# Kernel optimization log

Hardware: AMD Instinct MI355X
Metric: run time of the kernel (lower is better)

Reference implementation:

```python
import jax, jax.numpy as jnp
import numpy as np

D_MODEL = 512
N_HEADS = 8
D_HEAD = D_MODEL // N_HEADS
EPS = 1e-5


def layer_norm(x, g, b):
    mu = jnp.mean(x, axis=-1, keepdims=True)
    var = jnp.mean(jnp.square(x - mu), axis=-1, keepdims=True)
    return (x - mu) * jax.lax.rsqrt(var + EPS) * g + b


def setup_inputs() -> dict:
    key = jax.random.key(0)
    ks = jax.random.split(key, 8)
    B, L, D = 2, 4096, D_MODEL
    x = jax.random.normal(ks[0], (B, L, D), dtype=jnp.float32)
    # monotonically increasing event timestamps (hours)
    timestamps = jnp.sort(jax.random.uniform(ks[1], (B, L), dtype=jnp.float32) * 1000.0, axis=-1)
    mask = jnp.ones((B, L), dtype=jnp.float32)
    s = 0.02
    return {
        "x": x,
        "timestamps": timestamps,
        "mask": mask,
        "ln1_g": jnp.ones((D,), jnp.float32),
        "ln1_b": jnp.zeros((D,), jnp.float32),
        "w_qkv": jax.random.normal(ks[2], (3 * D, D), jnp.float32) * s,
        "w_out": jax.random.normal(ks[3], (D, D), jnp.float32) * s,
        "decay_rate": jnp.ones((N_HEADS,), jnp.float32) * 0.01,
        "ln2_g": jnp.ones((D,), jnp.float32),
        "ln2_b": jnp.zeros((D,), jnp.float32),
        "w_ff1": jax.random.normal(ks[4], (4 * D, D), jnp.float32) * s,
        "w_ff2": jax.random.normal(ks[5], (D, 4 * D), jnp.float32) * s,
    }


def reference(x, timestamps, mask, ln1_g, ln1_b, w_qkv, w_out, decay_rate, ln2_g, ln2_b, w_ff1, w_ff2):
    B, L, D = x.shape
    H, dh = N_HEADS, D_HEAD
    scale = dh ** (-0.5)

    xn = layer_norm(x, ln1_g, ln1_b)
    qkv = (xn @ w_qkv.T).reshape(B, L, 3, H, dh).transpose(2, 0, 3, 1, 4)  # [3,B,H,L,dh]
    q, k, v = qkv[0], qkv[1], qkv[2]

    attn = jnp.einsum("bhid,bhjd->bhij", q, k) * scale  # [B,H,L,L]

    # temporal-decay bias
    t_diff = jnp.abs(timestamps[:, None, :, None] - timestamps[:, None, None, :]) / 24.0  # [B,1,L,L]
    decay = jax.nn.softplus(decay_rate)[None, :, None, None]  # [1,H,1,1]
    attn = attn - decay * t_diff

    # causal mask
    causal = jnp.triu(jnp.ones((L, L), dtype=bool), k=1)
    attn = jnp.where(causal[None, None], -jnp.inf, attn)

    # padding mask over keys
    pad = (mask == 0)[:, None, None, :]  # [B,1,1,L]
    attn = jnp.where(pad, -jnp.inf, attn)

    attn = jax.nn.softmax(attn, axis=-1)
    out = jnp.einsum("bhij,bhjd->bhid", attn, v).transpose(0, 2, 1, 3).reshape(B, L, D)

    x = x + out @ w_out.T
    h = layer_norm(x, ln2_g, ln2_b)
    x = x + jax.nn.silu(h @ w_ff1.T) @ w_ff2.T
    return x
```

## Files before the change

### kernel.cpp

```cpp
#include <hip/hip_runtime.h>
#include <hip/hip_bf16.h>
#include <cmath>


#define L_SEQ 4096
#define D_MODEL 512
#define N_HEADS 8
#define D_HEAD 64
#define QKV_LD 1536

typedef __attribute__((ext_vector_type(8))) short bf16x8;
typedef __attribute__((ext_vector_type(4))) float f32x4;
typedef __attribute__((ext_vector_type(4))) unsigned u32x4;

__device__ __forceinline__ __hip_bfloat16 f2bf(float v) { return __float2bfloat16(v); }

__device__ __forceinline__ float exp2_raw(float x) {
  float r;
  asm("v_exp_f32 %0, %1" : "=v"(r) : "v"(x));
  return r;
}

__device__ __forceinline__ void gl_lds16(const __hip_bfloat16* g, __hip_bfloat16* l) {
  __builtin_amdgcn_global_load_lds((__attribute__((address_space(1))) void*)g,
                                   (__attribute__((address_space(3))) void*)l, 16, 0, 0);
}

__global__ __launch_bounds__(256) void cvt4b_kernel(const float* __restrict__ s0, __hip_bfloat16* __restrict__ d0,
                                                    const float* __restrict__ s1, __hip_bfloat16* __restrict__ d1,
                                                    const float* __restrict__ s2, __hip_bfloat16* __restrict__ d2,
                                                    const float* __restrict__ s3, __hip_bfloat16* __restrict__ d3,
                                                    const float* __restrict__ ts,
                                                    const float* __restrict__ mask,
                                                    const float* __restrict__ decay_rate,
                                                    float* __restrict__ biasH) {
  const int i = blockIdx.x * 256 + threadIdx.x;
  if (i < 786432) {
    const float* s;
    __hip_bfloat16* d;
    int off;
    if (i < 196608) { s = s0; d = d0; off = i; }
    else if (i < 262144) { s = s1; d = d1; off = i - 196608; }
    else if (i < 524288) { s = s2; d = d2; off = i - 262144; }
    else { s = s3; d = d3; off = i - 524288; }
    const float4 v = ((const float4*)s)[off];
    d[4 * off + 0] = f2bf(v.x);
    d[4 * off + 1] = f2bf(v.y);
    d[4 * off + 2] = f2bf(v.z);
    d[4 * off + 3] = f2bf(v.w);
  } else {
    const int idx = i - 786432;
    const int col = idx & 4095;
    const int h = (idx >> 12) & 7;
    const int b = idx >> 15;
    const float LOG2E = 1.4426950408889634f;
    const float dfac = log1pf(expf(decay_rate[h])) * (1.0f / 24.0f) * LOG2E;
    const float m = mask[b * 4096 + col];
    biasH[idx] = dfac * ts[b * 4096 + col] + (m != 0.f ? 0.f : -1e30f);
  }
}

__global__ __launch_bounds__(256) void ln_kernel(const float* __restrict__ x,
                                                 const float* __restrict__ g,
                                                 const float* __restrict__ b,
                                                 __hip_bfloat16* __restrict__ out) {
  const int row = blockIdx.x;
  const int t = threadIdx.x;
  const float* xr = x + (size_t)row * D_MODEL;
  float v0 = xr[t];
  float v1 = xr[t + 256];
  float s = v0 + v1;
  float qq = v0 * v0 + v1 * v1;
  for (int off = 32; off > 0; off >>= 1) {
    s += __shfl_xor(s, off);
    qq += __shfl_xor(qq, off);
  }
  __shared__ float red[8];
  const int wid = t >> 6;
  if ((t & 63) == 0) { red[wid] = s; red[4 + wid] = qq; }
  __syncthreads();
  s = red[0] + red[1] + red[2] + red[3];
  qq = red[4] + red[5] + red[6] + red[7];
  const float mu = s * (1.0f / 512.0f);
  const float var = fmaxf(qq * (1.0f / 512.0f) - mu * mu, 0.0f);
  const float rstd = rsqrtf(var + 1e-5f);
  __hip_bfloat16* orow = out + (size_t)row * D_MODEL;
  orow[t] = f2bf((v0 - mu) * rstd * g[t] + b[t]);
  orow[t + 256] = f2bf((v1 - mu) * rstd * g[t + 256] + b[t + 256]);
}

template <int EPI>
__global__ __launch_bounds__(256) void gemm_kernel(const __hip_bfloat16* __restrict__ A,
                                                   const __hip_bfloat16* __restrict__ B,
                                                   int M, int N, int K,
                                                   __hip_bfloat16* __restrict__ vtout,
                                                   void* __restrict__ C) {
  __shared__ __align__(16) __hip_bfloat16 As[2][128 * 32];
  __shared__ __align__(16) __hip_bfloat16 Bs[2][128 * 32];
  const int tid = threadIdx.x;
  const int lane = tid & 63, w = tid >> 6;
  const int m0 = blockIdx.y * 128, n0 = blockIdx.x * 128;
  const int wm = (w >> 1) * 64, wn = (w & 1) * 64;
  const int r = lane & 15, q = lane >> 4;

  f32x4 acc[4][4];
  const f32x4 zz = {0.f, 0.f, 0.f, 0.f};
  for (int i = 0; i < 4; i++)
    for (int j = 0; j < 4; j++) acc[i][j] = zz;

  const int c0 = tid, c1 = 256 + tid;
  const int row0 = c0 >> 2, kb0 = (c0 & 3) * 8;
  const int row1 = c1 >> 2, kb1 = (c1 & 3) * 8;

#define GEMM_STAGE(k0, buf)                                                     \
  do {                                                                          \
    gl_lds16(A + (size_t)(m0 + row0) * K + ((k0) + kb0), &As[buf][c0 * 8]);     \
    gl_lds16(B + (size_t)(n0 + row0) * K + ((k0) + kb0), &Bs[buf][c0 * 8]);     \
    gl_lds16(A + (size_t)(m0 + row1) * K + ((k0) + kb1), &As[buf][c1 * 8]);     \
    gl_lds16(B + (size_t)(n0 + row1) * K + ((k0) + kb1), &Bs[buf][c1 * 8]);     \
  } while (0)

  GEMM_STAGE(0, 0);
  const int niter = K >> 5;
  for (int it = 0; it < niter; it++) {
    const int cur = it & 1;
    if (it + 1 < niter) {
      GEMM_STAGE((it + 1) << 5, cur ^ 1);
      asm volatile("s_waitcnt vmcnt(4)" ::: "memory");
    } else {
      asm volatile("s_waitcnt vmcnt(0)" ::: "memory");
    }
    __builtin_amdgcn_s_barrier();
    bf16x8 af[4], bfr[4];
    for (int mi = 0; mi < 4; mi++)
      af[mi] = *(const bf16x8*)(&As[cur][(wm + mi * 16 + r) * 32 + q * 8]);
    for (int ni = 0; ni < 4; ni++)
      bfr[ni] = *(const bf16x8*)(&Bs[cur][(wn + ni * 16 + r) * 32 + q * 8]);
    for (int mi = 0; mi < 4; mi++)
      for (int ni = 0; ni < 4; ni++)
        acc[mi][ni] = __builtin_amdgcn_mfma_f32_16x16x32_bf16(af[mi], bfr[ni], acc[mi][ni], 0, 0, 0);
    __builtin_amdgcn_s_barrier();
  }
#undef GEMM_STAGE

  for (int mi = 0; mi < 4; mi++)
    for (int ni = 0; ni < 4; ni++)
      for (int j = 0; j < 4; j++) {
        const int gm = m0 + wm + mi * 16 + q * 4 + j;
        const int gn = n0 + wn + ni * 16 + r;
        float v = acc[mi][ni][j];
        const size_t idx = (size_t)gm * N + gn;
        if (EPI == 0) {
          ((__hip_bfloat16*)C)[idx] = f2bf(v);
        } else if (EPI == 2) {
          v = v / (1.0f + expf(-v));
          ((__hip_bfloat16*)C)[idx] = f2bf(v);
        } else {
          if (n0 < 1024) {
            ((__hip_bfloat16*)C)[idx] = f2bf(v);
          } else {
            const int bb = gm >> 12, ll = gm & 4095;
            const int hd = gn - 1024;
            const int kin = ll & 63;
            const int sl = (kin & 0x23) | ((kin & 0x10) >> 2) | ((kin & 0x0c) << 1);
            vtout[(size_t)(bb * 512 + hd) * 4096 + (ll & ~63) + sl] = f2bf(v);
          }
        }
      }
}

__global__ __launch_bounds__(256) void gemm_res64_kernel(const __hip_bfloat16* __restrict__ A,
                                                         const __hip_bfloat16* __restrict__ B,
                                                         int M, int N, int K,
                                                         const float* __restrict__ aux,
                                                         float* __restrict__ C) {
  __shared__ __align__(16) __hip_bfloat16 As[2][64 * 32];
  __shared__ __align__(16) __hip_bfloat16 Bs[2][128 * 32];
  const int tid = threadIdx.x;
  const int lane = tid & 63, w = tid >> 6;
  const int m0 = blockIdx.y * 64, n0 = blockIdx.x * 128;
  const int wm = (w >> 1) * 32, wn = (w & 1) * 64;
  const int r = lane & 15, q = lane >> 4;

  f32x4 acc[2][4];
  const f32x4 zz = {0.f, 0.f, 0.f, 0.f};
  for (int i = 0; i < 2; i++)
    for (int j = 0; j < 4; j++) acc[i][j] = zz;

  const int rowA = tid >> 2, kbA = (tid & 3) * 8;
  const int c0 = tid, c1 = 256 + tid;
  const int rowB0 = c0 >> 2, kb0 = (c0 & 3) * 8;
  const int rowB1 = c1 >> 2, kb1 = (c1 & 3) * 8;

#define GEMM_STAGE64(k0, buf)                                                    \
  do {                                                                           \
    gl_lds16(A + (size_t)(m0 + rowA) * K + ((k0) + kbA), &As[buf][tid * 8]);     \
    gl_lds16(B + (size_t)(n0 + rowB0) * K + ((k0) + kb0), &Bs[buf][c0 * 8]);     \
    gl_lds16(B + (size_t)(n0 + rowB1) * K + ((k0) + kb1), &Bs[buf][c1 * 8]);     \
  } while (0)

  GEMM_STAGE64(0, 0);
  const int niter = K >> 5;
  for (int it = 0; it < niter; it++) {
    const int cur = it & 1;
    if (it + 1 < niter) {
      GEMM_STAGE64((it + 1) << 5, cur ^ 1);
      asm volatile("s_waitcnt vmcnt(3)" ::: "memory");
    } else {
      asm volatile("s_waitcnt vmcnt(0)" ::: "memory");
    }
    __builtin_amdgcn_s_barrier();
    bf16x8 af[2], bfr[4];
    for (int mi = 0; mi < 2; mi++)
      af[mi] = *(const bf16x8*)(&As[cur][(wm + mi * 16 + r) * 32 + q * 8]);
    for (int ni = 0; ni < 4; ni++)
      bfr[ni] = *(const bf16x8*)(&Bs[cur][(wn + ni * 16 + r) * 32 + q * 8]);
    for (int mi = 0; mi < 2; mi++)
      for (int ni = 0; ni < 4; ni++)
        acc[mi][ni] = __builtin_amdgcn_mfma_f32_16x16x32_bf16(af[mi], bfr[ni], acc[mi][ni], 0, 0, 0);
    __builtin_amdgcn_s_barrier();
  }
#undef GEMM_STAGE64

  for (int mi = 0; mi < 2; mi++)
    for (int ni = 0; ni < 4; ni++)
      for (int j = 0; j < 4; j++) {
        const int gm = m0 + wm + mi * 16 + q * 4 + j;
        const int gn = n0 + wn + ni * 16 + r;
        const size_t idx = (size_t)gm * N + gn;
        C[idx] = acc[mi][ni][j] + aux[idx];
      }
}

__device__ __forceinline__ void stage_kv128(int w, int lane, int key0,
                                            const __hip_bfloat16* __restrict__ Kg,
                                            const __hip_bfloat16* __restrict__ Vg,
                                            __hip_bfloat16* Ks, __hip_bfloat16* Vs) {
  const int krow_in = lane >> 3;
  const int kcs = (lane & 7) ^ krow_in;
  const int vrow_in = lane >> 4;
  const int vch = lane & 15;
#pragma unroll
  for (int ii = 0; ii < 2; ii++) {
    const int i = w * 2 + ii;
    const int krow = i * 8 + krow_in;
    gl_lds16(Kg + (size_t)(key0 + krow) * QKV_LD + kcs * 8, Ks + i * 512 + lane * 8);
    const int vrow = i * 4 + vrow_in;
    const int vcs = vch ^ (vrow & 7);
    gl_lds16(Vg + (size_t)vrow * L_SEQ + key0 + vcs * 8, Vs + i * 512 + lane * 8);
  }
}

template <bool CAUSAL>
__device__ __forceinline__ void attn_tile128(int key0, int lw0, int r, int q,
                                             const __hip_bfloat16* Ks,
                                             const __hip_bfloat16* Vs,
                                             const float* biasLds,
                                             float scale2,
                                             const bf16x8& qf0, const bf16x8& qf1,
                                             const bf16x8& onesf,
                                             f32x4* o, f32x4& ls) {
  const int r7 = r & 7;
  const f32x4 zz = {0.f, 0.f, 0.f, 0.f};
  f32x4 bias4[8];
#pragma unroll
  for (int hc = 0; hc < 8; hc++)
    bias4[hc] = *(const f32x4*)(biasLds + key0 + hc * 16 + q * 4);
  f32x4 s[8];
  __builtin_amdgcn_s_setprio(1);
#pragma unroll
  for (int hc = 0; hc < 8; hc++) {
    const __hip_bfloat16* kr = Ks + (hc * 16 + r) * 64;
    bf16x8 k0 = *(const bf16x8*)(kr + ((q ^ r7) * 8));
    bf16x8 k1 = *(const bf16x8*)(kr + (((q + 4) ^ r7) * 8));
    f32x4 a = zz;
    a = __builtin_amdgcn_mfma_f32_16x16x32_bf16(k0, qf0, a, 0, 0, 0);
    a = __builtin_amdgcn_mfma_f32_16x16x32_bf16(k1, qf1, a, 0, 0, 0);
    s[hc] = a;
  }
  __builtin_amdgcn_s_setprio(0);
  float p[8][4];
#pragma unroll
  for (int hc = 0; hc < 8; hc++)
#pragma unroll
    for (int j = 0; j < 4; j++) {
      float pv = exp2_raw(fmaf(s[hc][j], scale2, bias4[hc][j]));
      if (CAUSAL) pv = (key0 + hc * 16 + q * 4 + j <= lw0 + r) ? pv : 0.f;
      p[hc][j] = pv;
    }
  bf16x8 pa[4];
#pragma unroll
  for (int kc = 0; kc < 4; kc++) {
    u32x4 pw;
    unsigned w0, w1, w2, w3;
    asm("v_cvt_pk_bf16_f32 %0, %1, %2" : "=v"(w0) : "v"(p[2 * kc][0]), "v"(p[2 * kc][1]));
    asm("v_cvt_pk_bf16_f32 %0, %1, %2" : "=v"(w1) : "v"(p[2 * kc][2]), "v"(p[2 * kc][3]));
    asm("v_cvt_pk_bf16_f32 %0, %1, %2" : "=v"(w2) : "v"(p[2 * kc + 1][0]), "v"(p[2 * kc + 1][1]));
    asm("v_cvt_pk_bf16_f32 %0, %1, %2" : "=v"(w3) : "v"(p[2 * kc + 1][2]), "v"(p[2 * kc + 1][3]));
    pw[0] = w0; pw[1] = w1; pw[2] = w2; pw[3] = w3;
    pa[kc] = *(bf16x8*)&pw;
  }
  __builtin_amdgcn_s_setprio(1);
#pragma unroll
  for (int kc = 0; kc < 4; kc++) {
#pragma unroll
    for (int c = 0; c < 4; c++) {
      const __hip_bfloat16* vr = Vs + (c * 16 + r) * 128 + (((kc * 4 + q) ^ r7) * 8);
      bf16x8 vf = *(const bf16x8*)vr;
      o[c] = __builtin_amdgcn_mfma_f32_16x16x32_bf16(pa[kc], vf, o[c], 0, 0, 0);
    }
    ls = __builtin_amdgcn_mfma_f32_16x16x32_bf16(pa[kc], onesf, ls, 0, 0, 0);
  }
  __builtin_amdgcn_s_setprio(0);
}

__global__ __launch_bounds__(512, 4) void attn_kernel(const __hip_bfloat16* __restrict__ qkv,
                                                      const __hip_bfloat16* __restrict__ vt,
                                                      const float* __restrict__ biasH,
                                                      __hip_bfloat16* __restrict__ out) {
  const int blk = blockIdx.x;
  const int bh = blk & 15;
  const int pr = blk >> 4;
  const int b = bh >> 3, h = bh & 7;
  const int tid = threadIdx.x, lane = tid & 63, w = tid >> 6;
  const int grp = w >> 2, wg = w & 3;
  const int qi = grp ? (63 - pr) : pr;
  const int l0 = qi * 64;
  const int lw0 = l0 + wg * 16;
  const int r = lane & 15, q = lane >> 4;

  __shared__ __align__(16) __hip_bfloat16 Ksm[2][128 * 64];
  __shared__ __align__(16) __hip_bfloat16 Vsm[2][64 * 128];
  __shared__ __align__(16) float biasLds[4096];

  const float LOG2E = 1.4426950408889634f;
  const float scale2 = 0.125f * LOG2E;

  const __hip_bfloat16* Kg = qkv + (size_t)b * L_SEQ * QKV_LD + 512 + h * 64;
  const __hip_bfloat16* Vg = vt + (size_t)bh * 64 * L_SEQ;
  const float* biasHp = biasH + (size_t)bh * L_SEQ;

  stage_kv128(w, lane, 0, Kg, Vg, Ksm[0], Vsm[0]);
#pragma unroll
  for (int ii = 0; ii < 2; ii++) {
    const int fo = (w * 2 + ii) * 256;
    gl_lds16((const __hip_bfloat16*)(biasHp + fo + lane * 4),
             (__hip_bfloat16*)(biasLds + fo + lane * 4));
  }

  bf16x8 qf0, qf1;
  {
    const __hip_bfloat16* qrow = qkv + (size_t)(b * L_SEQ + lw0 + r) * QKV_LD + h * 64 + q * 8;
    qf0 = *(const bf16x8*)qrow;
    qf1 = *(const bf16x8*)(qrow + 32);
  }

  const f32x4 zz = {0.f, 0.f, 0.f, 0.f};
  f32x4 o[4];
  for (int c = 0; c < 4; c++) o[c] = zz;
  f32x4 ls = zz;

  bf16x8 onesf;
  for (int i = 0; i < 8; i++) ((short*)&onesf)[i] = (short)0x3F80;

  const int ntA = (pr >> 1) + 1;
  const int ntB = ((63 - pr) >> 1) + 1;
  const int nt = grp ? ntB : ntA;

  for (int t = 0; t < ntB; t++) {
    const int cur = t & 1;
    if (t + 1 < ntB) {
      stage_kv128(w, lane, (t + 1) << 7, Kg, Vg, Ksm[cur ^ 1], Vsm[cur ^ 1]);
      asm volatile("s_waitcnt vmcnt(4)" ::: "memory");
    } else {
      asm volatile("s_waitcnt vmcnt(0)" ::: "memory");
    }
    __builtin_amdgcn_s_barrier();
    if (t < nt) {
      if (t == nt - 1)
        attn_tile128<true>(t << 7, lw0, r, q, Ksm[cur], Vsm[cur], biasLds, scale2, qf0, qf1,
                           onesf, o, ls);
      else
        attn_tile128<false>(t << 7, lw0, r, q, Ksm[cur], Vsm[cur], biasLds, scale2, qf0, qf1,
                            onesf, o, ls);
    }
    __builtin_amdgcn_s_barrier();
  }

  float invj[4];
  for (int j = 0; j < 4; j++) invj[j] = 1.0f / ls[j];
  for (int c = 0; c < 4; c++)
    for (int j = 0; j < 4; j++) {
      const int rowg = lw0 + q * 4 + j;
      out[(size_t)(b * L_SEQ + rowg) * D_MODEL + h * 64 + c * 16 + r] = f2bf(o[c][j] * invj[j]);
    }
}

extern "C" void kernel_launch(void* const* d_in, const int* in_sizes, int n_in,
                              void* d_out, int out_size, void* d_ws, size_t ws_size,
                              hipStream_t stream) {
  const float* x = (const float*)d_in[0];
  const float* ts = (const float*)d_in[1];
  const float* mask = (const float*)d_in[2];
  const float* ln1_g = (const float*)d_in[3];
  const float* ln1_b = (const float*)d_in[4];
  const float* w_qkv = (const float*)d_in[5];
  const float* w_out = (const float*)d_in[6];
  const float* decay = (const float*)d_in[7];
  const float* ln2_g = (const float*)d_in[8];
  const float* ln2_b = (const float*)d_in[9];
  const float* w_ff1 = (const float*)d_in[10];
  const float* w_ff2 = (const float*)d_in[11];

  char* ws = (char*)d_ws;
  __hip_bfloat16* wqkv_b = (__hip_bfloat16*)(ws + 0);
  __hip_bfloat16* wout_b = (__hip_bfloat16*)(ws + 1572864);
  __hip_bfloat16* wff1_b = (__hip_bfloat16*)(ws + 2097152);
  __hip_bfloat16* wff2_b = (__hip_bfloat16*)(ws + 4194304);
  __hip_bfloat16* xn = (__hip_bfloat16*)(ws + 6291456);
  __hip_bfloat16* qkv = (__hip_bfloat16*)(ws + 14680064);
  __hip_bfloat16* attnout = (__hip_bfloat16*)(ws + 39845888);
  __hip_bfloat16* h = attnout;
  __hip_bfloat16* ff1out = (__hip_bfloat16*)(ws + 6291456);
  float* x2 = (float*)(ws + 48234496);
  float* biasH = (float*)(ws + 48234496);
  __hip_bfloat16* vt = (__hip_bfloat16*)(ws + 48496640);
  float* out = (float*)d_out;

  const int M = 2 * L_SEQ;

  cvt4b_kernel<<<dim3(3328), dim3(256), 0, stream>>>(w_qkv, wqkv_b, w_out, wout_b,
                                                     w_ff1, wff1_b, w_ff2, wff2_b,
                                                     ts, mask, decay, biasH);

  ln_kernel<<<dim3(M), dim3(256), 0, stream>>>(x, ln1_g, ln1_b, xn);
  gemm_kernel<4><<<dim3(12, 64), dim3(256), 0, stream>>>(xn, wqkv_b, M, 1536, 512, vt, qkv);
  attn_kernel<<<dim3(512), dim3(512), 0, stream>>>(qkv, vt, biasH, attnout);
  gemm_res64_kernel<<<dim3(4, 128), dim3(256), 0, stream>>>(attnout, wout_b, M, 512, 512, x, x2);
  ln_kernel<<<dim3(M), dim3(256), 0, stream>>>(x2, ln2_g, ln2_b, h);
  gemm_kernel<2><<<dim3(16, 64), dim3(256), 0, stream>>>(h, wff1_b, M, 2048, 512, nullptr, ff1out);
  gemm_res64_kernel<<<dim3(4, 128), dim3(256), 0, stream>>>(ff1out, wff2_b, M, 512, 2048, x2, out);
}
```

Before: 267.8 us.

## Triple-buffer GEMM LDS staging and fuse first layernorm into prep kernel

Both GEMM kernels move from double to triple buffering of shared-memory tiles. The next-next tile is now prefetched after the MFMA block, which cuts one barrier per iteration and leaves more time to hide global-load latency. The first layernorm is also merged into the weight-conversion and bias prep kernel as extra blocks, which removes one launch. The extra LDS may lower occupancy, and the single remaining barrier has to guard the reuse of each buffer correctly.

```diff
diff --git a/kernel.cpp b/kernel.cpp
--- a/kernel.cpp
+++ b/kernel.cpp
@@ -26,37 +26,67 @@
                                    (__attribute__((address_space(3))) void*)l, 16, 0, 0);
 }
 
-__global__ __launch_bounds__(256) void cvt4b_kernel(const float* __restrict__ s0, __hip_bfloat16* __restrict__ d0,
-                                                    const float* __restrict__ s1, __hip_bfloat16* __restrict__ d1,
-                                                    const float* __restrict__ s2, __hip_bfloat16* __restrict__ d2,
-                                                    const float* __restrict__ s3, __hip_bfloat16* __restrict__ d3,
-                                                    const float* __restrict__ ts,
-                                                    const float* __restrict__ mask,
-                                                    const float* __restrict__ decay_rate,
-                                                    float* __restrict__ biasH) {
-  const int i = blockIdx.x * 256 + threadIdx.x;
-  if (i < 786432) {
-    const float* s;
-    __hip_bfloat16* d;
-    int off;
-    if (i < 196608) { s = s0; d = d0; off = i; }
-    else if (i < 262144) { s = s1; d = d1; off = i - 196608; }
-    else if (i < 524288) { s = s2; d = d2; off = i - 262144; }
-    else { s = s3; d = d3; off = i - 524288; }
-    const float4 v = ((const float4*)s)[off];
-    d[4 * off + 0] = f2bf(v.x);
-    d[4 * off + 1] = f2bf(v.y);
-    d[4 * off + 2] = f2bf(v.z);
-    d[4 * off + 3] = f2bf(v.w);
+__global__ __launch_bounds__(256) void prep_kernel(const float* __restrict__ s0, __hip_bfloat16* __restrict__ d0,
+                                                   const float* __restrict__ s1, __hip_bfloat16* __restrict__ d1,
+                                                   const float* __restrict__ s2, __hip_bfloat16* __restrict__ d2,
+                                                   const float* __restrict__ s3, __hip_bfloat16* __restrict__ d3,
+                                                   const float* __restrict__ ts,
+                                                   const float* __restrict__ mask,
+                                                   const float* __restrict__ decay_rate,
+                                                   float* __restrict__ biasH,
+                                                   const float* __restrict__ x,
+                                                   const float* __restrict__ ln1_g,
+                                                   const float* __restrict__ ln1_b,
+                                                   __hip_bfloat16* __restrict__ xn) {
+  if (blockIdx.x < 3328) {
+    const int i = blockIdx.x * 256 + threadIdx.x;
+    if (i < 786432) {
+      const float* s;
+      __hip_bfloat16* d;
+      int off;
+      if (i < 196608) { s = s0; d = d0; off = i; }
+      else if (i < 262144) { s = s1; d = d1; off = i - 196608; }
+      else if (i < 524288) { s = s2; d = d2; off = i - 262144; }
+      else { s = s3; d = d3; off = i - 524288; }
+      const float4 v = ((const float4*)s)[off];
+      d[4 * off + 0] = f2bf(v.x);
+      d[4 * off + 1] = f2bf(v.y);
+      d[4 * off + 2] = f2bf(v.z);
+      d[4 * off + 3] = f2bf(v.w);
+    } else {
+      const int idx = i - 786432;
+      const int col = idx & 4095;
+      const int h = (idx >> 12) & 7;
+      const int b = idx >> 15;
+      const float LOG2E = 1.4426950408889634f;
+      const float dfac = log1pf(expf(decay_rate[h])) * (1.0f / 24.0f) * LOG2E;
+      const float m = mask[b * 4096 + col];
+      biasH[idx] = dfac * ts[b * 4096 + col] + (m != 0.f ? 0.f : -1e30f);
+    }
   } else {
-    const int idx = i - 786432;
-    const int col = idx & 4095;
-    const int h = (idx >> 12) & 7;
-    const int b = idx >> 15;
-    const float LOG2E = 1.4426950408889634f;
-    const float dfac = log1pf(expf(decay_rate[h])) * (1.0f / 24.0f) * LOG2E;
-    const float m = mask[b * 4096 + col];
-    biasH[idx] = dfac * ts[b * 4096 + col] + (m != 0.f ? 0.f : -1e30f);
+    const int row = blockIdx.x - 3328;
+    const int t = threadIdx.x;
+    const float* xr = x + (size_t)row * D_MODEL;
+    float v0 = xr[t];
+    float v1 = xr[t + 256];
+    float s = v0 + v1;
+    float qq = v0 * v0 + v1 * v1;
+    for (int off = 32; off > 0; off >>= 1) {
+      s += __shfl_xor(s, off);
+      qq += __shfl_xor(qq, off);
+    }
+    __shared__ float red[8];
+    const int wid = t >> 6;
+    if ((t & 63) == 0) { red[wid] = s; red[4 + wid] = qq; }
+    __syncthreads();
+    s = red[0] + red[1] + red[2] + red[3];
+    qq = red[4] + red[5] + red[6] + red[7];
+    const float mu = s * (1.0f / 512.0f);
+    const float var = fmaxf(qq * (1.0f / 512.0f) - mu * mu, 0.0f);
+    const float rstd = rsqrtf(var + 1e-5f);
+    __hip_bfloat16* orow = xn + (size_t)row * D_MODEL;
+    orow[t] = f2bf((v0 - mu) * rstd * ln1_g[t] + ln1_b[t]);
+    orow[t + 256] = f2bf((v1 - mu) * rstd * ln1_g[t + 256] + ln1_b[t + 256]);
   }
 }
 
@@ -95,8 +125,8 @@
                                                    int M, int N, int K,
                                                    __hip_bfloat16* __restrict__ vtout,
                                                    void* __restrict__ C) {
-  __shared__ __align__(16) __hip_bfloat16 As[2][128 * 32];
-  __shared__ __align__(16) __hip_bfloat16 Bs[2][128 * 32];
+  __shared__ __align__(16) __hip_bfloat16 As[3][128 * 32];
+  __shared__ __align__(16) __hip_bfloat16 Bs[3][128 * 32];
   const int tid = threadIdx.x;
   const int lane = tid & 63, w = tid >> 6;
   const int m0 = blockIdx.y * 128, n0 = blockIdx.x * 128;
@@ -120,17 +150,17 @@
     gl_lds16(B + (size_t)(n0 + row1) * K + ((k0) + kb1), &Bs[buf][c1 * 8]);     \
   } while (0)
 
+  const int niter = K >> 5;
   GEMM_STAGE(0, 0);
-  const int niter = K >> 5;
+  if (niter > 1) GEMM_STAGE(32, 1);
   for (int it = 0; it < niter; it++) {
-    const int cur = it & 1;
+    const int cur = it % 3;
+    __builtin_amdgcn_s_barrier();
     if (it + 1 < niter) {
-      GEMM_STAGE((it + 1) << 5, cur ^ 1);
       asm volatile("s_waitcnt vmcnt(4)" ::: "memory");
     } else {
       asm volatile("s_waitcnt vmcnt(0)" ::: "memory");
     }
-    __builtin_amdgcn_s_barrier();
     bf16x8 af[4], bfr[4];
     for (int mi = 0; mi < 4; mi++)
       af[mi] = *(const bf16x8*)(&As[cur][(wm + mi * 16 + r) * 32 + q * 8]);
@@ -139,7 +169,7 @@
     for (int mi = 0; mi < 4; mi++)
       for (int ni = 0; ni < 4; ni++)
         acc[mi][ni] = __builtin_amdgcn_mfma_f32_16x16x32_bf16(af[mi], bfr[ni], acc[mi][ni], 0, 0, 0);
-    __builtin_amdgcn_s_barrier();
+    if (it + 2 < niter) GEMM_STAGE((it + 2) << 5, (it + 2) % 3);
   }
 #undef GEMM_STAGE
 
@@ -174,8 +204,8 @@
                                                          int M, int N, int K,
                                                          const float* __restrict__ aux,
                                                          float* __restrict__ C) {
-  __shared__ __align__(16) __hip_bfloat16 As[2][64 * 32];
-  __shared__ __align__(16) __hip_bfloat16 Bs[2][128 * 32];
+  __shared__ __align__(16) __hip_bfloat16 As[3][64 * 32];
+  __shared__ __align__(16) __hip_bfloat16 Bs[3][128 * 32];
   const int tid = threadIdx.x;
   const int lane = tid & 63, w = tid >> 6;
   const int m0 = blockIdx.y * 64, n0 = blockIdx.x * 128;
@@ -199,17 +229,17 @@
     gl_lds16(B + (size_t)(n0 + rowB1) * K + ((k0) + kb1), &Bs[buf][c1 * 8]);     \
   } while (0)
 
+  const int niter = K >> 5;
   GEMM_STAGE64(0, 0);
-  const int niter = K >> 5;
+  if (niter > 1) GEMM_STAGE64(32, 1);
   for (int it = 0; it < niter; it++) {
-    const int cur = it & 1;
+    const int cur = it % 3;
+    __builtin_amdgcn_s_barrier();
     if (it + 1 < niter) {
-      GEMM_STAGE64((it + 1) << 5, cur ^ 1);
       asm volatile("s_waitcnt vmcnt(3)" ::: "memory");
     } else {
       asm volatile("s_waitcnt vmcnt(0)" ::: "memory");
     }
-    __builtin_amdgcn_s_barrier();
     bf16x8 af[2], bfr[4];
     for (int mi = 0; mi < 2; mi++)
       af[mi] = *(const bf16x8*)(&As[cur][(wm + mi * 16 + r) * 32 + q * 8]);
@@ -218,7 +248,7 @@
     for (int mi = 0; mi < 2; mi++)
       for (int ni = 0; ni < 4; ni++)
         acc[mi][ni] = __builtin_amdgcn_mfma_f32_16x16x32_bf16(af[mi], bfr[ni], acc[mi][ni], 0, 0, 0);
-    __builtin_amdgcn_s_barrier();
+    if (it + 2 < niter) GEMM_STAGE64((it + 2) << 5, (it + 2) % 3);
   }
 #undef GEMM_STAGE64
 
@@ -429,11 +459,11 @@
 
   const int M = 2 * L_SEQ;
 
-  cvt4b_kernel<<<dim3(3328), dim3(256), 0, stream>>>(w_qkv, wqkv_b, w_out, wout_b,
+  prep_kernel<<<dim3(11520), dim3(256), 0, stream>>>(w_qkv, wqkv_b, w_out, wout_b,
                                                      w_ff1, wff1_b, w_ff2, wff2_b,
-                                                     ts, mask, decay, biasH);
-
-  ln_kernel<<<dim3(M), dim3(256), 0, stream>>>(x, ln1_g, ln1_b, xn);
+                                                     ts, mask, decay, biasH,
+                                                     x, ln1_g, ln1_b, xn);
+
   gemm_kernel<4><<<dim3(12, 64), dim3(256), 0, stream>>>(xn, wqkv_b, M, 1536, 512, vt, qkv);
   attn_kernel<<<dim3(512), dim3(512), 0, stream>>>(qkv, vt, biasH, attnout);
   gemm_res64_kernel<<<dim3(4, 128), dim3(256), 0, stream>>>(attnout, wout_b, M, 512, 512, x, x2);
```

Result: slower. 273.9 us (+2.3%).
